# Optimization experiments

Hardware: AMD Instinct MI355X
Metric: run time of the kernel (lower is better)

Reference implementation:

```python
import jax, jax.numpy as jnp
import numpy as np

NEG = -1e9  # safe stand-in for log(0) in the one-hot initial state distribution


def setup_inputs() -> dict:
    key = jax.random.key(0)
    k1, k2 = jax.random.split(key)
    Q, S = 128, 96
    B, T = 2048, 48
    # log-space transition weights A[q, s, q']
    A = jax.random.normal(k1, (Q, S, Q), dtype=jnp.float32)
    # batch of symbol sequences
    xs = jax.random.randint(k2, (B, T), 0, S, dtype=jnp.int64)
    return {"A": A, "xs": xs}


def reference(A, xs):
    """FSA phonotactics log-likelihood: HMM-style forward algorithm in the log semiring.

    A:  [Q, S, Q] log-space weights (normalized per source state so that
        sum over (S, Q') of exp(A[q]) == 1, as in A_and_final_normalized).
    xs: [B, T] int symbol ids.
    Returns per-sequence log-likelihood [B] (final weights are all-ones).
    """
    Q, S, _ = A.shape
    B, T = xs.shape
    # normalize: each source state's outgoing mass sums to 1 in exp-space
    logZ = jax.nn.logsumexp(A.reshape(Q, -1), axis=-1)      # [Q]
    A_norm = A - logZ[:, None, None]                         # [Q, S, Q]
    # init = one-hot on state 0 (log-space)
    log_alpha0 = jnp.full((B, Q), NEG, dtype=A.dtype).at[:, 0].set(0.0)

    def step(log_alpha, tok):
        # tok: [B]; gather per-symbol transition matrices: [Q, B, Q]
        M = A_norm[:, tok, :]
        # alpha'[b, q'] = logsumexp_q( alpha[b, q] + M[q, b, q'] )
        la = jax.nn.logsumexp(log_alpha.T[:, :, None] + M, axis=0)  # [B, Q]
        return la, None

    log_alpha, _ = jax.lax.scan(step, log_alpha0, xs.T)  # scan over time
    # final = all ones -> vv(alpha, final) = sum over states (logsumexp in log space)
    return jax.nn.logsumexp(log_alpha, axis=-1)  # [B]
```

## Files before the change

### kernel.cpp

```cpp
#include <hip/hip_runtime.h>

#define QN 128
#define SN 96
#define TN 48
#define ROWSTRIDE (SN * QN)
#define WT_BYTES ((size_t)SN * QN * QN * 2)
#define NSEG 6
#define SEGLEN (ROWSTRIDE / NSEG)
#define SHIFT 10.0f

__global__ __launch_bounds__(256)
void fsa_partial_sum(const float* __restrict__ A, float* __restrict__ part) {
    const int bid = blockIdx.x;
    const int q   = bid / NSEG;
    const int seg = bid % NSEG;
    const int tid = threadIdx.x;
    const float* base = A + (size_t)q * ROWSTRIDE + seg * SEGLEN + tid * 8;

    const float4 v0 = *reinterpret_cast<const float4*>(base);
    const float4 v1 = *reinterpret_cast<const float4*>(base + 4);
    float s = (__expf(v0.x - SHIFT) + __expf(v0.y - SHIFT)) +
              (__expf(v0.z - SHIFT) + __expf(v0.w - SHIFT)) +
              (__expf(v1.x - SHIFT) + __expf(v1.y - SHIFT)) +
              (__expf(v1.z - SHIFT) + __expf(v1.w - SHIFT));

    __shared__ float red[256];
    red[tid] = s;
    __syncthreads();
    #pragma unroll
    for (int o = 128; o > 0; o >>= 1) {
        if (tid < o) red[tid] += red[tid + o];
        __syncthreads();
    }
    if (tid == 0) part[bid] = red[0];
}

__global__ __launch_bounds__(256)
void fsa_write_bf16(const float* __restrict__ A, const float* __restrict__ part,
                    ushort* __restrict__ Wt) {
    const int bid = blockIdx.x;
    const int q   = bid / NSEG;
    const int seg = bid % NSEG;
    const int tid = threadIdx.x;

    float zs = 0.0f;
    #pragma unroll
    for (int j = 0; j < NSEG; ++j) zs += part[q * NSEG + j];
    const float logZ = SHIFT + __logf(zs);

    const int li = seg * SEGLEN + tid * 8;
    const float* src = A + (size_t)q * ROWSTRIDE + li;
    const int s  = li >> 7;
    const int qp = li & 127;

    uint u[4];
    #pragma unroll
    for (int e = 0; e < 4; ++e) {
        const float2 v = *reinterpret_cast<const float2*>(src + 2 * e);
        const float w0 = __expf(v.x - logZ);
        const float w1 = __expf(v.y - logZ);
        uint b0 = __float_as_uint(w0);
        uint b1 = __float_as_uint(w1);
        b0 = (b0 + 0x7fffu + ((b0 >> 16) & 1u)) >> 16;
        b1 = (b1 + 0x7fffu + ((b1 >> 16) & 1u)) >> 16;
        u[e] = b0 | (b1 << 16);
    }
    uint4* dst = reinterpret_cast<uint4*>(
        Wt + (size_t)s * (QN * QN) + (size_t)q * QN + qp);
    *dst = make_uint4(u[0], u[1], u[2], u[3]);
}

__global__ __launch_bounds__(256)
void fsa_forward_bf16(const ushort* __restrict__ Wt, const int* __restrict__ xs,
                      float* __restrict__ out, int B) {
    const int wv   = threadIdx.x >> 6;
    const int lane = threadIdx.x & 63;
    const int b    = blockIdx.x * 4 + wv;
    if (b >= B) return;

    __shared__ __align__(16) float sp[4][QN];
    __shared__ int stok[4][TN];

    if (lane < TN) stok[wv][lane] = xs[b * TN + lane];
    sp[wv][2 * lane]     = (lane == 0) ? 1.0f : 0.0f;
    sp[wv][2 * lane + 1] = 0.0f;
    float c = 0.0f;

    for (int t = 0; t < TN; ++t) {
        const int tok = stok[wv][t];
        const uint* wp = reinterpret_cast<const uint*>(Wt + ((size_t)tok << 14)) + lane;

        float a0 = 0.0f, a1 = 0.0f;
        #pragma unroll 8
        for (int k = 0; k < QN; k += 4) {
            const float4 pv = *reinterpret_cast<const float4*>(&sp[wv][k]);
            const uint w0 = wp[(k + 0) * 64];
            const uint w1 = wp[(k + 1) * 64];
            const uint w2 = wp[(k + 2) * 64];
            const uint w3 = wp[(k + 3) * 64];
            a0 = fmaf(pv.x, __uint_as_float(w0 << 16), a0);
            a1 = fmaf(pv.x, __uint_as_float(w0 & 0xffff0000u), a1);
            a0 = fmaf(pv.y, __uint_as_float(w1 << 16), a0);
            a1 = fmaf(pv.y, __uint_as_float(w1 & 0xffff0000u), a1);
            a0 = fmaf(pv.z, __uint_as_float(w2 << 16), a0);
            a1 = fmaf(pv.z, __uint_as_float(w2 & 0xffff0000u), a1);
            a0 = fmaf(pv.w, __uint_as_float(w3 << 16), a0);
            a1 = fmaf(pv.w, __uint_as_float(w3 & 0xffff0000u), a1);
        }

        if ((t & 7) == 7) {
            float s2 = a0 + a1;
            #pragma unroll
            for (int off = 32; off > 0; off >>= 1) s2 += __shfl_xor(s2, off, 64);
            c += __logf(s2);
            const float inv = 1.0f / s2;
            a0 *= inv; a1 *= inv;
        }
        *reinterpret_cast<float2*>(&sp[wv][2 * lane]) = make_float2(a0, a1);
    }
    if (lane == 0) out[b] = c;
}


__global__ __launch_bounds__(256)
void fsa_normalize(float* __restrict__ A) {
    const int q   = blockIdx.x;
    const int tid = threadIdx.x;
    float* row = A + (size_t)q * ROWSTRIDE;
    __shared__ float red[256];
    float mx = -1e30f;
    for (int i = tid; i < ROWSTRIDE; i += 256) mx = fmaxf(mx, row[i]);
    red[tid] = mx;
    __syncthreads();
    #pragma unroll
    for (int s = 128; s > 0; s >>= 1) {
        if (tid < s) red[tid] = fmaxf(red[tid], red[tid + s]);
        __syncthreads();
    }
    const float bmax = red[0];
    __syncthreads();
    float sum = 0.0f;
    for (int i = tid; i < ROWSTRIDE; i += 256) sum += expf(row[i] - bmax);
    red[tid] = sum;
    __syncthreads();
    #pragma unroll
    for (int s = 128; s > 0; s >>= 1) {
        if (tid < s) red[tid] += red[tid + s];
        __syncthreads();
    }
    const float logZ = bmax + logf(red[0]);
    for (int i = tid; i < ROWSTRIDE; i += 256) row[i] = expf(row[i] - logZ);
}

__global__ __launch_bounds__(128)
void fsa_forward(const float* __restrict__ W, const int* __restrict__ xs,
                 float* __restrict__ out) {
    const int b = blockIdx.x;
    const int q = threadIdx.x;
    __shared__ __align__(16) float sp[QN];
    __shared__ float red[QN];
    __shared__ int  stok[TN];
    if (q < TN) stok[q] = xs[b * TN + q];
    sp[q] = (q == 0) ? 1.0f : 0.0f;
    float c = 0.0f;
    __syncthreads();
    for (int t = 0; t < TN; ++t) {
        const int tok = stok[t];
        const float* wp = W + ((size_t)tok << 7) + q;
        float a0 = 0.f, a1 = 0.f, a2 = 0.f, a3 = 0.f;
        #pragma unroll 8
        for (int k = 0; k < QN; k += 4) {
            const float4 pv = *reinterpret_cast<const float4*>(&sp[k]);
            a0 = fmaf(pv.x, wp[0 * ROWSTRIDE], a0);
            a1 = fmaf(pv.y, wp[1 * ROWSTRIDE], a1);
            a2 = fmaf(pv.z, wp[2 * ROWSTRIDE], a2);
            a3 = fmaf(pv.w, wp[3 * ROWSTRIDE], a3);
            wp += 4 * ROWSTRIDE;
        }
        float acc = (a0 + a1) + (a2 + a3);
        __syncthreads();
        if ((t & 7) == 7) {
            red[q] = acc;
            __syncthreads();
            #pragma unroll
            for (int s = 64; s > 0; s >>= 1) {
                if (q < s) red[q] += red[q + s];
                __syncthreads();
            }
            const float m = red[0];
            c += logf(m);
            sp[q] = acc * (1.0f / m);
            __syncthreads();
        } else {
            sp[q] = acc;
            __syncthreads();
        }
    }
    if (q == 0) out[b] = c;
}


extern "C" void kernel_launch(void* const* d_in, const int* in_sizes, int n_in,
                              void* d_out, int out_size, void* d_ws, size_t ws_size,
                              hipStream_t stream) {
    float* A      = (float*)d_in[0];
    const int* xs = (const int*)d_in[1];
    float* out    = (float*)d_out;
    const int B   = in_sizes[1] / TN;

    const size_t need = WT_BYTES + (size_t)QN * NSEG * sizeof(float);
    if (ws_size >= need) {
        ushort* Wt  = (ushort*)d_ws;
        float* part = (float*)((unsigned char*)d_ws + WT_BYTES);
        hipLaunchKernelGGL(fsa_partial_sum, dim3(QN * NSEG), dim3(256), 0, stream,
                           A, part);
        hipLaunchKernelGGL(fsa_write_bf16, dim3(QN * NSEG), dim3(256), 0, stream,
                           A, part, Wt);
        hipLaunchKernelGGL(fsa_forward_bf16, dim3((B + 3) / 4), dim3(256), 0, stream,
                           Wt, xs, out, B);
        return;
    }
    hipLaunchKernelGGL(fsa_normalize, dim3(QN), dim3(256), 0, stream, A);
    hipLaunchKernelGGL(fsa_forward, dim3(B), dim3(QN), 0, stream, A, xs, out);
}
```

Baseline: 178.5 us.

## Quantize normalized transition weights to 8-bit with a global log scale

Preprocessing now also computes per-row maxima and stores the normalized exponentiated weights as unsigned 8-bit fixed point, using one global scale taken from the largest normalized weight. Four source states are packed into each 32-bit word. The forward kernel unpacks the bytes to floats and adds the accumulated log scale back at the end. Weight traffic per step is half that of the bf16 version, and renormalization now runs every 4 steps to avoid overflow. The cost is a large loss of precision: small weights round to zero or to a few levels, which risks accuracy failures.

```diff
diff --git a/kernel.cpp b/kernel.cpp
--- a/kernel.cpp
+++ b/kernel.cpp
@@ -4,13 +4,20 @@
 #define SN 96
 #define TN 48
 #define ROWSTRIDE (SN * QN)
-#define WT_BYTES ((size_t)SN * QN * QN * 2)
 #define NSEG 6
 #define SEGLEN (ROWSTRIDE / NSEG)
 #define SHIFT 10.0f
-
-__global__ __launch_bounds__(256)
-void fsa_partial_sum(const float* __restrict__ A, float* __restrict__ part) {
+#define LOG255 5.5412635451584258f
+
+#define U8_BYTES ((size_t)SN * QN * QN)
+#define PART_OFF (U8_BYTES)
+#define RMAX_OFF (PART_OFF + (size_t)QN * NSEG * 4)
+#define LSC_OFF  (RMAX_OFF + (size_t)QN * NSEG * 4)
+#define WS_NEED  (LSC_OFF + 16)
+
+__global__ __launch_bounds__(256)
+void fsa_stats(const float* __restrict__ A, float* __restrict__ part,
+               float* __restrict__ rowmax) {
     const int bid = blockIdx.x;
     const int q   = bid / NSEG;
     const int seg = bid % NSEG;
@@ -23,56 +30,86 @@
               (__expf(v0.z - SHIFT) + __expf(v0.w - SHIFT)) +
               (__expf(v1.x - SHIFT) + __expf(v1.y - SHIFT)) +
               (__expf(v1.z - SHIFT) + __expf(v1.w - SHIFT));
-
-    __shared__ float red[256];
-    red[tid] = s;
+    float m = fmaxf(fmaxf(fmaxf(v0.x, v0.y), fmaxf(v0.z, v0.w)),
+                    fmaxf(fmaxf(v1.x, v1.y), fmaxf(v1.z, v1.w)));
+
+    __shared__ float reds[256];
+    __shared__ float redm[256];
+    reds[tid] = s; redm[tid] = m;
     __syncthreads();
     #pragma unroll
     for (int o = 128; o > 0; o >>= 1) {
-        if (tid < o) red[tid] += red[tid + o];
-        __syncthreads();
-    }
-    if (tid == 0) part[bid] = red[0];
-}
-
-__global__ __launch_bounds__(256)
-void fsa_write_bf16(const float* __restrict__ A, const float* __restrict__ part,
-                    ushort* __restrict__ Wt) {
+        if (tid < o) {
+            reds[tid] += reds[tid + o];
+            redm[tid] = fmaxf(redm[tid], redm[tid + o]);
+        }
+        __syncthreads();
+    }
+    if (tid == 0) { part[bid] = reds[0]; rowmax[bid] = redm[0]; }
+}
+
+__global__ __launch_bounds__(256)
+void fsa_write_u8(const float* __restrict__ A, const float* __restrict__ part,
+                  const float* __restrict__ rowmax, uint* __restrict__ U,
+                  float* __restrict__ logsc_p) {
     const int bid = blockIdx.x;
-    const int q   = bid / NSEG;
+    const int kq  = bid / NSEG;
     const int seg = bid % NSEG;
     const int tid = threadIdx.x;
 
-    float zs = 0.0f;
-    #pragma unroll
-    for (int j = 0; j < NSEG; ++j) zs += part[q * NSEG + j];
-    const float logZ = SHIFT + __logf(zs);
+    __shared__ float lz[QN];
+    __shared__ float dl[QN];
+    if (tid < QN) {
+        float z = 0.0f, rm = -1e30f;
+        #pragma unroll
+        for (int j = 0; j < NSEG; ++j) {
+            z  += part[tid * NSEG + j];
+            rm  = fmaxf(rm, rowmax[tid * NSEG + j]);
+        }
+        const float l = SHIFT + __logf(z);
+        lz[tid] = l;
+        dl[tid] = rm - l;
+    }
+    __syncthreads();
+    #pragma unroll
+    for (int o = 64; o > 0; o >>= 1) {
+        if (tid < o) dl[tid] = fmaxf(dl[tid], dl[tid + o]);
+        __syncthreads();
+    }
+    const float glob = dl[0];
+    if (bid == 0 && tid == 0) logsc_p[0] = glob - LOG255;
 
     const int li = seg * SEGLEN + tid * 8;
-    const float* src = A + (size_t)q * ROWSTRIDE + li;
     const int s  = li >> 7;
     const int qp = li & 127;
 
-    uint u[4];
-    #pragma unroll
-    for (int e = 0; e < 4; ++e) {
-        const float2 v = *reinterpret_cast<const float2*>(src + 2 * e);
-        const float w0 = __expf(v.x - logZ);
-        const float w1 = __expf(v.y - logZ);
-        uint b0 = __float_as_uint(w0);
-        uint b1 = __float_as_uint(w1);
-        b0 = (b0 + 0x7fffu + ((b0 >> 16) & 1u)) >> 16;
-        b1 = (b1 + 0x7fffu + ((b1 >> 16) & 1u)) >> 16;
-        u[e] = b0 | (b1 << 16);
-    }
-    uint4* dst = reinterpret_cast<uint4*>(
-        Wt + (size_t)s * (QN * QN) + (size_t)q * QN + qp);
-    *dst = make_uint4(u[0], u[1], u[2], u[3]);
-}
-
-__global__ __launch_bounds__(256)
-void fsa_forward_bf16(const ushort* __restrict__ Wt, const int* __restrict__ xs,
-                      float* __restrict__ out, int B) {
+    uint d0 = 0, d1 = 0, d2 = 0, d3 = 0, d4 = 0, d5 = 0, d6 = 0, d7 = 0;
+    #pragma unroll
+    for (int j = 0; j < 4; ++j) {
+        const int k = 4 * kq + j;
+        const float* src = A + (size_t)k * ROWSTRIDE + li;
+        const float off = lz[k] + glob;
+        const float4 v0 = *reinterpret_cast<const float4*>(src);
+        const float4 v1 = *reinterpret_cast<const float4*>(src + 4);
+        const int sh = 8 * j;
+        d0 |= ((uint)(255.0f * __expf(v0.x - off) + 0.5f)) << sh;
+        d1 |= ((uint)(255.0f * __expf(v0.y - off) + 0.5f)) << sh;
+        d2 |= ((uint)(255.0f * __expf(v0.z - off) + 0.5f)) << sh;
+        d3 |= ((uint)(255.0f * __expf(v0.w - off) + 0.5f)) << sh;
+        d4 |= ((uint)(255.0f * __expf(v1.x - off) + 0.5f)) << sh;
+        d5 |= ((uint)(255.0f * __expf(v1.y - off) + 0.5f)) << sh;
+        d6 |= ((uint)(255.0f * __expf(v1.z - off) + 0.5f)) << sh;
+        d7 |= ((uint)(255.0f * __expf(v1.w - off) + 0.5f)) << sh;
+    }
+    uint* dst = U + (size_t)s * (QN * QN / 4) + kq * QN + qp;
+    *reinterpret_cast<uint4*>(dst)     = make_uint4(d0, d1, d2, d3);
+    *reinterpret_cast<uint4*>(dst + 4) = make_uint4(d4, d5, d6, d7);
+}
+
+__global__ __launch_bounds__(256)
+void fsa_forward_u8(const uint* __restrict__ U, const int* __restrict__ xs,
+                    const float* __restrict__ logsc_p, float* __restrict__ out,
+                    int B) {
     const int wv   = threadIdx.x >> 6;
     const int lane = threadIdx.x & 63;
     const int b    = blockIdx.x * 4 + wv;
@@ -84,41 +121,42 @@
     if (lane < TN) stok[wv][lane] = xs[b * TN + lane];
     sp[wv][2 * lane]     = (lane == 0) ? 1.0f : 0.0f;
     sp[wv][2 * lane + 1] = 0.0f;
+    const float logsc = logsc_p[0];
     float c = 0.0f;
 
     for (int t = 0; t < TN; ++t) {
-        const int tok = stok[wv][t];
-        const uint* wp = reinterpret_cast<const uint*>(Wt + ((size_t)tok << 14)) + lane;
+        int tok = __builtin_amdgcn_readfirstlane(stok[wv][t]);
+        tok = (tok < 0) ? 0 : ((tok >= SN) ? (SN - 1) : tok);
+        const uint2* wp = reinterpret_cast<const uint2*>(
+            U + (size_t)tok * (QN * QN / 4)) + lane;
 
         float a0 = 0.0f, a1 = 0.0f;
         #pragma unroll 8
-        for (int k = 0; k < QN; k += 4) {
-            const float4 pv = *reinterpret_cast<const float4*>(&sp[wv][k]);
-            const uint w0 = wp[(k + 0) * 64];
-            const uint w1 = wp[(k + 1) * 64];
-            const uint w2 = wp[(k + 2) * 64];
-            const uint w3 = wp[(k + 3) * 64];
-            a0 = fmaf(pv.x, __uint_as_float(w0 << 16), a0);
-            a1 = fmaf(pv.x, __uint_as_float(w0 & 0xffff0000u), a1);
-            a0 = fmaf(pv.y, __uint_as_float(w1 << 16), a0);
-            a1 = fmaf(pv.y, __uint_as_float(w1 & 0xffff0000u), a1);
-            a0 = fmaf(pv.z, __uint_as_float(w2 << 16), a0);
-            a1 = fmaf(pv.z, __uint_as_float(w2 & 0xffff0000u), a1);
-            a0 = fmaf(pv.w, __uint_as_float(w3 << 16), a0);
-            a1 = fmaf(pv.w, __uint_as_float(w3 & 0xffff0000u), a1);
-        }
-
-        if ((t & 7) == 7) {
+        for (int kq = 0; kq < 32; ++kq) {
+            const uint2 w   = wp[kq * 64];
+            const float4 pv = *reinterpret_cast<const float4*>(&sp[wv][4 * kq]);
+            a0 = fmaf(pv.x, (float)( w.x        & 0xffu), a0);
+            a0 = fmaf(pv.y, (float)((w.x >>  8) & 0xffu), a0);
+            a0 = fmaf(pv.z, (float)((w.x >> 16) & 0xffu), a0);
+            a0 = fmaf(pv.w, (float)( w.x >> 24         ), a0);
+            a1 = fmaf(pv.x, (float)( w.y        & 0xffu), a1);
+            a1 = fmaf(pv.y, (float)((w.y >>  8) & 0xffu), a1);
+            a1 = fmaf(pv.z, (float)((w.y >> 16) & 0xffu), a1);
+            a1 = fmaf(pv.w, (float)( w.y >> 24         ), a1);
+        }
+
+        if ((t & 3) == 3) {
             float s2 = a0 + a1;
             #pragma unroll
             for (int off = 32; off > 0; off >>= 1) s2 += __shfl_xor(s2, off, 64);
+            s2 = fmaxf(s2, 1e-30f);
             c += __logf(s2);
             const float inv = 1.0f / s2;
             a0 *= inv; a1 *= inv;
         }
         *reinterpret_cast<float2*>(&sp[wv][2 * lane]) = make_float2(a0, a1);
     }
-    if (lane == 0) out[b] = c;
+    if (lane == 0) out[b] = c + (float)TN * logsc;
 }
 
 
@@ -208,16 +246,18 @@
     float* out    = (float*)d_out;
     const int B   = in_sizes[1] / TN;
 
-    const size_t need = WT_BYTES + (size_t)QN * NSEG * sizeof(float);
-    if (ws_size >= need) {
-        ushort* Wt  = (ushort*)d_ws;
-        float* part = (float*)((unsigned char*)d_ws + WT_BYTES);
-        hipLaunchKernelGGL(fsa_partial_sum, dim3(QN * NSEG), dim3(256), 0, stream,
-                           A, part);
-        hipLaunchKernelGGL(fsa_write_bf16, dim3(QN * NSEG), dim3(256), 0, stream,
-                           A, part, Wt);
-        hipLaunchKernelGGL(fsa_forward_bf16, dim3((B + 3) / 4), dim3(256), 0, stream,
-                           Wt, xs, out, B);
+    if (ws_size >= WS_NEED) {
+        unsigned char* ws = (unsigned char*)d_ws;
+        uint*  U8      = (uint*)ws;
+        float* part    = (float*)(ws + PART_OFF);
+        float* rowmax  = (float*)(ws + RMAX_OFF);
+        float* logsc_p = (float*)(ws + LSC_OFF);
+        hipLaunchKernelGGL(fsa_stats, dim3(QN * NSEG), dim3(256), 0, stream,
+                           A, part, rowmax);
+        hipLaunchKernelGGL(fsa_write_u8, dim3((QN / 4) * NSEG), dim3(256), 0, stream,
+                           A, part, rowmax, U8, logsc_p);
+        hipLaunchKernelGGL(fsa_forward_u8, dim3((B + 3) / 4), dim3(256), 0, stream,
+                           U8, xs, logsc_p, out, B);
         return;
     }
     hipLaunchKernelGGL(fsa_normalize, dim3(QN), dim3(256), 0, stream, A);
```

New measurement: 162.2 us. 1.1x faster.
